# Performance work log

Measured on AMD Instinct MI355X. Metric: run time of the kernel, lower is better.

## Reference

```python
import jax, jax.numpy as jnp
import numpy as np

V, D, H, L, B, T = 32000, 1024, 16, 4, 2, 2048
DH = D // H
F = 4 * D
EPS = 1e-5


def setup_inputs() -> dict:
    key = jax.random.key(0)
    ks = jax.random.split(key, 16)
    s = 0.02
    n = lambda k, shape: (jax.random.normal(k, shape, jnp.float32) * s)
    inp = {
        "idx": jax.random.randint(ks[0], (B, T), 0, V, dtype=jnp.int64),
        "tok_emb": n(ks[1], (V, D)),
        "pos_emb": n(ks[2], (1, T, D)),
        # per-layer stacked params; Linear weights stored as (in, out)
        "Wq": n(ks[3], (L, D, D)), "bq": jnp.zeros((L, D)),
        "Wk": n(ks[4], (L, D, D)), "bk": jnp.zeros((L, D)),
        "Wv": n(ks[5], (L, D, D)), "bv": jnp.zeros((L, D)),
        "Wo": n(ks[6], (L, D, D)), "bo": jnp.zeros((L, D)),
        "ln1_g": jnp.ones((L, D)), "ln1_b": jnp.zeros((L, D)),
        "W1": n(ks[7], (L, D, F)), "b1": jnp.zeros((L, F)),
        "W2": n(ks[8], (L, F, D)), "b2": jnp.zeros((L, D)),
        "ln2_g": jnp.ones((L, D)), "ln2_b": jnp.zeros((L, D)),
        "lnf_g": jnp.ones((D,)), "lnf_b": jnp.zeros((D,)),
        "lm_W": n(ks[9], (D, V)),
    }
    return inp


def _ln(x, g, b):
    m = jnp.mean(x, axis=-1, keepdims=True)
    v = jnp.mean(jnp.square(x - m), axis=-1, keepdims=True)
    return (x - m) * jax.lax.rsqrt(v + EPS) * g + b


def _band_attn(x, Wq, bq, Wk, bk, Wv, bv, Wo, bo):
    # width-3 causal band: query t attends to keys {t, t-1, t-2}
    b_, t_, _ = x.shape
    q = (x @ Wq + bq).reshape(b_, t_, H, DH)
    k = (x @ Wk + bk).reshape(b_, t_, H, DH)
    v = (x @ Wv + bv).reshape(b_, t_, H, DH)

    def shift(a, o):  # align key at position t-o with query t
        return jnp.pad(a, ((0, 0), (o, 0), (0, 0), (0, 0)))[:, :t_]

    ks_ = jnp.stack([shift(k, o) for o in range(3)], axis=-2)  # (B,T,H,3,DH)
    vs_ = jnp.stack([shift(v, o) for o in range(3)], axis=-2)
    scale = 1.0 / np.sqrt(DH)
    scores = jnp.einsum('bthd,bthod->btho', q, ks_) * scale       # (B,T,H,3)
    pos = jnp.arange(t_)[None, :, None, None]
    off = jnp.arange(3)[None, None, None, :]
    scores = jnp.where(pos >= off, scores, -jnp.inf)
    p = jax.nn.softmax(scores, axis=-1)
    y = jnp.einsum('btho,bthod->bthd', p, vs_).reshape(b_, t_, D)
    return y @ Wo + bo


def reference(idx, tok_emb, pos_emb, Wq, bq, Wk, bk, Wv, bv, Wo, bo,
              ln1_g, ln1_b, W1, b1, W2, b2, ln2_g, ln2_b, lnf_g, lnf_b, lm_W):
    t_ = idx.shape[1]
    x = tok_emb[idx] + pos_emb[:, :t_, :]
    for i in range(L):
        h = _ln(x, ln1_g[i], ln1_b[i])
        x = x + _band_attn(h, Wq[i], bq[i], Wk[i], bk[i], Wv[i], bv[i], Wo[i], bo[i])
        h = _ln(x, ln2_g[i], ln2_b[i])
        h = jax.nn.gelu(h @ W1[i] + b1[i], approximate=False) @ W2[i] + b2[i]
        x = x + h
    x = _ln(x, lnf_g, lnf_b)
    logits = x @ lm_W
    return logits
```

## Files before the change

kernel.cpp:

```cpp
#include <hip/hip_runtime.h>
#include <cstdint>
#include <cstddef>

#define MROWS   4096
#define TSEQ    2048
#define DMODEL  1024
#define NHEAD   16
#define FFN     4096
#define NVOCAB  32000
#define NLAYER  4

typedef float  f32x4  __attribute__((ext_vector_type(4)));
typedef __bf16 bf16x8 __attribute__((ext_vector_type(8)));

#define VMCNT(n) asm volatile("s_waitcnt vmcnt(" #n ")" ::: "memory")
#define LGKM0()  asm volatile("s_waitcnt lgkmcnt(0)" ::: "memory")

__device__ __forceinline__ unsigned short f2bf(float f) {
    unsigned u = __builtin_bit_cast(unsigned, f);
    u += 0x7fffu + ((u >> 16) & 1u);
    return (unsigned short)(u >> 16);
}
__device__ __forceinline__ float bf2f(unsigned short u) {
    return __builtin_bit_cast(float, (unsigned)u << 16);
}

__device__ __forceinline__ float gelu_exact(float v) {
    return 0.5f * v * (1.0f + erff(v * 0.7071067811865476f));
}

__global__ __launch_bounds__(256) void embed_kernel(const int* __restrict__ idx,
                                                    const float* __restrict__ tok,
                                                    const float* __restrict__ pos,
                                                    float* __restrict__ x) {
    int row = blockIdx.x, tid = threadIdx.x;
    int token = idx[row];
    int t = row & (TSEQ - 1);
    float4 a = ((const float4*)(tok + (size_t)token * DMODEL))[tid];
    float4 p = ((const float4*)(pos + (size_t)t * DMODEL))[tid];
    a.x += p.x; a.y += p.y; a.z += p.z; a.w += p.w;
    ((float4*)(x + (size_t)row * DMODEL))[tid] = a;
}

__global__ __launch_bounds__(256) void ln_kernel(const float* __restrict__ x,
                                                 const float* __restrict__ g,
                                                 const float* __restrict__ b,
                                                 unsigned short* __restrict__ out) {
    int row = blockIdx.x, tid = threadIdx.x;
    float4 v = ((const float4*)(x + (size_t)row * DMODEL))[tid];
    float s1 = v.x + v.y + v.z + v.w;
    float s2 = v.x * v.x + v.y * v.y + v.z * v.z + v.w * v.w;
    for (int s = 32; s; s >>= 1) { s1 += __shfl_xor(s1, s); s2 += __shfl_xor(s2, s); }
    __shared__ float red[8];
    int lane = tid & 63, w = tid >> 6;
    if (lane == 0) { red[w] = s1; red[4 + w] = s2; }
    __syncthreads();
    s1 = red[0] + red[1] + red[2] + red[3];
    s2 = red[4] + red[5] + red[6] + red[7];
    float mean = s1 * (1.0f / DMODEL);
    float var  = s2 * (1.0f / DMODEL) - mean * mean;
    float rs   = rsqrtf(var + 1e-5f);
    float4 gv = ((const float4*)g)[tid];
    float4 bv = ((const float4*)b)[tid];
    size_t o = (size_t)row * DMODEL + tid * 4;
    out[o + 0] = f2bf((v.x - mean) * rs * gv.x + bv.x);
    out[o + 1] = f2bf((v.y - mean) * rs * gv.y + bv.y);
    out[o + 2] = f2bf((v.z - mean) * rs * gv.z + bv.z);
    out[o + 3] = f2bf((v.w - mean) * rs * gv.w + bv.w);
}

__global__ __launch_bounds__(256) void transpose_bf16(const float* __restrict__ W,
                                                      unsigned short* __restrict__ WT,
                                                      int K, int ldW) {
    __shared__ float tile[64][65];
    int n0 = blockIdx.x * 64, k0 = blockIdx.y * 64;
    int tid = threadIdx.x;
    int lr4 = tid & 15;
    int rw  = tid >> 4;
#pragma unroll
    for (int p = 0; p < 4; ++p) {
        int k = rw + p * 16;
        float4 v = *(const float4*)(W + (size_t)(k0 + k) * ldW + n0 + lr4 * 4);
        tile[k][lr4 * 4 + 0] = v.x;
        tile[k][lr4 * 4 + 1] = v.y;
        tile[k][lr4 * 4 + 2] = v.z;
        tile[k][lr4 * 4 + 3] = v.w;
    }
    __syncthreads();
    int kc = tid & 15;
    int nr = tid >> 4;
#pragma unroll
    for (int p = 0; p < 4; ++p) {
        int n = nr + p * 16;
        ushort4 o;
        o.x = f2bf(tile[kc * 4 + 0][n]);
        o.y = f2bf(tile[kc * 4 + 1][n]);
        o.z = f2bf(tile[kc * 4 + 2][n]);
        o.w = f2bf(tile[kc * 4 + 3][n]);
        *(ushort4*)(WT + (size_t)(n0 + n) * K + k0 + kc * 4) = o;
    }
}

__global__ __launch_bounds__(256) void transpose_qkv(const float* __restrict__ Wq,
                                                     const float* __restrict__ Wk,
                                                     const float* __restrict__ Wv,
                                                     unsigned short* __restrict__ WT) {
    __shared__ float tile[64][65];
    const float* W = (blockIdx.z == 0) ? Wq : (blockIdx.z == 1) ? Wk : Wv;
    unsigned short* dst = WT + (size_t)blockIdx.z * DMODEL * DMODEL;
    int n0 = blockIdx.x * 64, k0 = blockIdx.y * 64;
    int tid = threadIdx.x;
    int lr4 = tid & 15, rw = tid >> 4;
#pragma unroll
    for (int p = 0; p < 4; ++p) {
        int k = rw + p * 16;
        float4 v = *(const float4*)(W + (size_t)(k0 + k) * DMODEL + n0 + lr4 * 4);
        tile[k][lr4 * 4 + 0] = v.x;
        tile[k][lr4 * 4 + 1] = v.y;
        tile[k][lr4 * 4 + 2] = v.z;
        tile[k][lr4 * 4 + 3] = v.w;
    }
    __syncthreads();
    int kc = tid & 15, nr = tid >> 4;
#pragma unroll
    for (int p = 0; p < 4; ++p) {
        int n = nr + p * 16;
        ushort4 o;
        o.x = f2bf(tile[kc * 4 + 0][n]);
        o.y = f2bf(tile[kc * 4 + 1][n]);
        o.z = f2bf(tile[kc * 4 + 2][n]);
        o.w = f2bf(tile[kc * 4 + 3][n]);
        *(ushort4*)(dst + (size_t)(n0 + n) * DMODEL + k0 + kc * 4) = o;
    }
}

__global__ __launch_bounds__(256) void pack_qkv_bias(const float* __restrict__ bq,
                                                     const float* __restrict__ bk,
                                                     const float* __restrict__ bv,
                                                     float* __restrict__ dst) {
    int i = blockIdx.x * 256 + threadIdx.x;
    int l = i / 3072, c = i % 3072;
    float v = (c < 1024) ? bq[l * 1024 + c]
            : (c < 2048) ? bk[l * 1024 + c - 1024]
                         : bv[l * 1024 + c - 2048];
    dst[i] = v;
}

__global__ __launch_bounds__(256) void attn_kernel(const unsigned short* __restrict__ qkv,
                                                   unsigned short* __restrict__ y) {
    int wid  = (blockIdx.x * 256 + threadIdx.x) >> 6;
    int lane = threadIdx.x & 63;
    int h = wid & (NHEAD - 1);
    int row = wid >> 4;
    int t = row & (TSEQ - 1);
    const unsigned short* base = qkv + (size_t)row * 3072 + h * 64;
    float qd = bf2f(base[lane]);
    float d0 = qd * bf2f(base[1024 + lane]);
    float d1 = (t >= 1) ? qd * bf2f(base[1024 - 3072 + lane]) : 0.0f;
    float d2 = (t >= 2) ? qd * bf2f(base[1024 - 6144 + lane]) : 0.0f;
    for (int s = 32; s; s >>= 1) {
        d0 += __shfl_xor(d0, s); d1 += __shfl_xor(d1, s); d2 += __shfl_xor(d2, s);
    }
    d0 *= 0.125f; d1 *= 0.125f; d2 *= 0.125f;
    float m = d0;
    if (t >= 1) m = fmaxf(m, d1);
    if (t >= 2) m = fmaxf(m, d2);
    float p0 = expf(d0 - m);
    float p1 = (t >= 1) ? expf(d1 - m) : 0.0f;
    float p2 = (t >= 2) ? expf(d2 - m) : 0.0f;
    float den = p0 + p1 + p2;
    float v0 = bf2f(base[2048 + lane]);
    float v1 = (t >= 1) ? bf2f(base[2048 - 3072 + lane]) : 0.0f;
    float v2 = (t >= 2) ? bf2f(base[2048 - 6144 + lane]) : 0.0f;
    float yv = (p0 * v0 + p1 * v1 + p2 * v2) / den;
    y[(size_t)row * DMODEL + h * 64 + lane] = f2bf(yv);
}

template <int EPI>
__global__ __launch_bounds__(512, 2) void gemm256(const unsigned short* __restrict__ A,
                                                  const unsigned short* __restrict__ BT,
                                                  const float* __restrict__ bias,
                                                  const float* __restrict__ res,
                                                  float* __restrict__ outF,
                                                  unsigned short* __restrict__ outB,
                                                  int M, int N, int K, int ldc) {
    __shared__ unsigned short As[2][2][8192];
    __shared__ unsigned short Bs[2][2][8192];
    const int tid = threadIdx.x;
    const int lane = tid & 63, wid = tid >> 6;
    const int wr = wid >> 2, wc = wid & 3;
    const int lr = lane & 15, kq = lane >> 4;

    const int nbm = M >> 8;
    const int nwg = gridDim.x;
    int orig = blockIdx.x;
    int q8 = nwg >> 3, r8 = nwg & 7;
    int xcd = orig & 7, lin = orig >> 3;
    int wg = (xcd < r8 ? xcd * (q8 + 1) : r8 * (q8 + 1) + (xcd - r8) * q8) + lin;
    int bm = wg % nbm, bn = wg / nbm;

    const unsigned short* Ab = A + (size_t)bm * 256 * K;
    const unsigned short* Bb = BT + (size_t)bn * 256 * K;

    int sG0, sG1;
    {
        int pc0 = tid,        l0 = pc0 >> 3, s0 = pc0 & 7;
        int pc1 = 512 + tid,  l1 = pc1 >> 3, s1 = pc1 & 7;
        sG0 = (l0 * 2 + (s0 >> 2)) * K + (((s0 & 3) ^ (l0 & 3)) * 8);
        sG1 = (l1 * 2 + (s1 >> 2)) * K + (((s1 & 3) ^ (l1 & 3)) * 8);
    }

#define STAGE256(REGION, GBASE, TT, KH) do {                                                   \
    __builtin_amdgcn_global_load_lds(                                                          \
        (const __attribute__((address_space(1))) void*)((GBASE) + sG0 + (TT) * 64 + (KH) * 32),\
        (__attribute__((address_space(3))) void*)((REGION) + (size_t)tid * 8), 16, 0, 0);      \
    __builtin_amdgcn_global_load_lds(                                                          \
        (const __attribute__((address_space(1))) void*)((GBASE) + sG1 + (TT) * 64 + (KH) * 32),\
        (__attribute__((address_space(3))) void*)((REGION) + (size_t)(512 + tid) * 8), 16, 0, 0);\
} while (0)

    const int slot = ((lane & 1) << 2) | (kq ^ ((lr >> 1) & 3));
    const int laneOff = ((lr >> 1) << 6) + slot * 8;
    const int aBase = wr * 4096 + laneOff;
    const int bBase = wc * 2048 + laneOff;

    f32x4 acc[8][4] = {};
    const int nt = K >> 6;

    STAGE256(&As[0][0][0], Ab, 0, 0);
    STAGE256(&Bs[0][0][0], Bb, 0, 0);
    STAGE256(&As[0][1][0], Ab, 0, 1);
    STAGE256(&Bs[0][1][0], Bb, 0, 1);
    VMCNT(4);
    __builtin_amdgcn_s_barrier();

    for (int t = 0; t < nt; ++t) {
        const int buf = t & 1;
        const bool pf = (t + 1) < nt;
        const unsigned short* A0 = &As[buf][0][0];
        const unsigned short* A1 = &As[buf][1][0];
        const unsigned short* B0 = &Bs[buf][0][0];
        const unsigned short* B1 = &Bs[buf][1][0];
        unsigned short* nA0 = &As[buf ^ 1][0][0];
        unsigned short* nA1 = &As[buf ^ 1][1][0];
        unsigned short* nB0 = &Bs[buf ^ 1][0][0];
        unsigned short* nB1 = &Bs[buf ^ 1][1][0];

        bf16x8 a[8], b0, b1;

#pragma unroll
        for (int m = 0; m < 8; ++m) a[m] = *(const bf16x8*)(A0 + aBase + m * 512);
        b0 = *(const bf16x8*)(B0 + bBase + 0 * 512);
        b1 = *(const bf16x8*)(B0 + bBase + 1 * 512);
        if (pf) STAGE256(nA0, Ab, t + 1, 0);
        __builtin_amdgcn_s_barrier();
        LGKM0();
        __builtin_amdgcn_s_setprio(1);
#pragma unroll
        for (int m = 0; m < 8; ++m) {
            acc[m][0] = __builtin_amdgcn_mfma_f32_16x16x32_bf16(a[m], b0, acc[m][0], 0, 0, 0);
            acc[m][1] = __builtin_amdgcn_mfma_f32_16x16x32_bf16(a[m], b1, acc[m][1], 0, 0, 0);
        }
        __builtin_amdgcn_s_setprio(0);
        __builtin_amdgcn_s_barrier();

        b0 = *(const bf16x8*)(B0 + bBase + 2 * 512);
        b1 = *(const bf16x8*)(B0 + bBase + 3 * 512);
        if (pf) STAGE256(nB0, Bb, t + 1, 0);
        __builtin_amdgcn_s_barrier();
        LGKM0();
        __builtin_amdgcn_s_setprio(1);
#pragma unroll
        for (int m = 0; m < 8; ++m) {
            acc[m][2] = __builtin_amdgcn_mfma_f32_16x16x32_bf16(a[m], b0, acc[m][2], 0, 0, 0);
            acc[m][3] = __builtin_amdgcn_mfma_f32_16x16x32_bf16(a[m], b1, acc[m][3], 0, 0, 0);
        }
        __builtin_amdgcn_s_setprio(0);
        if (pf) VMCNT(4); else VMCNT(0);
        __builtin_amdgcn_s_barrier();

#pragma unroll
        for (int m = 0; m < 8; ++m) a[m] = *(const bf16x8*)(A1 + aBase + m * 512);
        b0 = *(const bf16x8*)(B1 + bBase + 0 * 512);
        b1 = *(const bf16x8*)(B1 + bBase + 1 * 512);
        if (pf) STAGE256(nA1, Ab, t + 1, 1);
        __builtin_amdgcn_s_barrier();
        LGKM0();
        __builtin_amdgcn_s_setprio(1);
#pragma unroll
        for (int m = 0; m < 8; ++m) {
            acc[m][0] = __builtin_amdgcn_mfma_f32_16x16x32_bf16(a[m], b0, acc[m][0], 0, 0, 0);
            acc[m][1] = __builtin_amdgcn_mfma_f32_16x16x32_bf16(a[m], b1, acc[m][1], 0, 0, 0);
        }
        __builtin_amdgcn_s_setprio(0);
        __builtin_amdgcn_s_barrier();

        b0 = *(const bf16x8*)(B1 + bBase + 2 * 512);
        b1 = *(const bf16x8*)(B1 + bBase + 3 * 512);
        if (pf) STAGE256(nB1, Bb, t + 1, 1);
        __builtin_amdgcn_s_barrier();
        LGKM0();
        __builtin_amdgcn_s_setprio(1);
#pragma unroll
        for (int m = 0; m < 8; ++m) {
            acc[m][2] = __builtin_amdgcn_mfma_f32_16x16x32_bf16(a[m], b0, acc[m][2], 0, 0, 0);
            acc[m][3] = __builtin_amdgcn_mfma_f32_16x16x32_bf16(a[m], b1, acc[m][3], 0, 0, 0);
        }
        __builtin_amdgcn_s_setprio(0);
        if (pf) VMCNT(4);
        __builtin_amdgcn_s_barrier();
    }

    const int row0 = bm * 256 + wr * 128;
    const int col0 = bn * 256 + wc * 64;
#pragma unroll
    for (int m = 0; m < 8; ++m) {
#pragma unroll
        for (int n = 0; n < 4; ++n) {
            int col = col0 + n * 16 + lr;
            int rbase = row0 + m * 16 + kq * 4;
            float bb = bias ? bias[col] : 0.0f;
#pragma unroll
            for (int j = 0; j < 4; ++j) {
                size_t off = (size_t)(rbase + j) * ldc + col;
                float v = acc[m][n][j] + bb;
                if (EPI == 1) v += res[off];
                if (EPI == 2)      outB[off] = f2bf(gelu_exact(v));
                else if (EPI == 3) outB[off] = f2bf(v);
                else               outF[off] = v;
            }
        }
    }
#undef STAGE256
}

template <int EPI>
__global__ __launch_bounds__(512, 4) void gemm128(const unsigned short* __restrict__ A,
                                                  const unsigned short* __restrict__ BT,
                                                  const float* __restrict__ bias,
                                                  const float* __restrict__ res,
                                                  float* __restrict__ outF,
                                                  unsigned short* __restrict__ outB,
                                                  int M, int N, int K, int ldc) {
    __shared__ unsigned short As[4][128 * 32];
    __shared__ unsigned short Bs[4][128 * 32];
    const int tid = threadIdx.x;
    const int lane = tid & 63, wid = tid >> 6;
    const int wr = wid >> 2, wc = wid & 3;
    const int lr = lane & 15, kq = lane >> 4;

    const int nbm = M >> 7;
    const int nwg = gridDim.x;
    int orig = blockIdx.x;
    int q8 = nwg >> 3, r8 = nwg & 7;
    int xcd = orig & 7, lin = orig >> 3;
    int wg = (xcd < r8 ? xcd * (q8 + 1) : r8 * (q8 + 1) + (xcd - r8) * q8) + lin;
    int bm = wg % nbm, bn = wg / nbm;

    const unsigned short* Ab = A + (size_t)bm * 128 * K;
    const unsigned short* Bb = BT + (size_t)bn * 128 * K;

    int sOff;
    {
        int l0 = tid >> 3, s0 = tid & 7;
        sOff = (l0 * 2 + (s0 >> 2)) * K + (((s0 & 3) ^ (l0 & 3)) * 8);
    }

#define STAGE_AB128(T) do {                                                                    \
    __builtin_amdgcn_global_load_lds(                                                          \
        (const __attribute__((address_space(1))) void*)(Ab + sOff + (T) * 32),                 \
        (__attribute__((address_space(3))) void*)(&As[(T) & 3][0] + (size_t)tid * 8), 16, 0, 0); \
    __builtin_amdgcn_global_load_lds(                                                          \
        (const __attribute__((address_space(1))) void*)(Bb + sOff + (T) * 32),                 \
        (__attribute__((address_space(3))) void*)(&Bs[(T) & 3][0] + (size_t)tid * 8), 16, 0, 0); \
} while (0)

    const int slot = ((lane & 1) << 2) | (kq ^ ((lr >> 1) & 3));
    const int laneOff = ((lr >> 1) << 6) + slot * 8;
    int aOff[4], bOff[2];
#pragma unroll
    for (int m = 0; m < 4; ++m) aOff[m] = wr * 2048 + m * 512 + laneOff;
#pragma unroll
    for (int n = 0; n < 2; ++n) bOff[n] = wc * 1024 + n * 512 + laneOff;

    f32x4 acc[4][2] = {};
    const int nt = K >> 5;

    STAGE_AB128(0); STAGE_AB128(1); STAGE_AB128(2);

#define GTILE128(T, WN, PF) do {                                                               \
    VMCNT(WN);                                                                                 \
    __builtin_amdgcn_s_barrier();                                                              \
    const unsigned short* sA_ = &As[(T) & 3][0];                                               \
    const unsigned short* sB_ = &Bs[(T) & 3][0];                                               \
    bf16x8 bfr[2], af[4];                                                                      \
    _Pragma("unroll") for (int n = 0; n < 2; ++n) bfr[n] = *(const bf16x8*)(sB_ + bOff[n]);    \
    _Pragma("unroll") for (int m = 0; m < 4; ++m) af[m] = *(const bf16x8*)(sA_ + aOff[m]);     \
    if (PF) STAGE_AB128((T) + 3);                                                              \
    __builtin_amdgcn_s_setprio(1);                                                             \
    _Pragma("unroll") for (int m = 0; m < 4; ++m)                                              \
        _Pragma("unroll") for (int n = 0; n < 2; ++n)                                          \
            acc[m][n] = __builtin_amdgcn_mfma_f32_16x16x32_bf16(af[m], bfr[n], acc[m][n], 0, 0, 0); \
    __builtin_amdgcn_s_setprio(0);                                                             \
} while (0)

    int t = 0;
    for (; t < nt - 3; ++t) GTILE128(t, 4, true);
    GTILE128(t, 4, false); ++t;
    GTILE128(t, 2, false); ++t;
    GTILE128(t, 0, false);

    const int row0 = bm * 128 + wr * 64;
    const int col0 = bn * 128 + wc * 32;
#pragma unroll
    for (int m = 0; m < 4; ++m) {
#pragma unroll
        for (int n = 0; n < 2; ++n) {
            int col = col0 + n * 16 + lr;
            int rbase = row0 + m * 16 + kq * 4;
            float bb = bias ? bias[col] : 0.0f;
#pragma unroll
            for (int j = 0; j < 4; ++j) {
                size_t off = (size_t)(rbase + j) * ldc + col;
                float v = acc[m][n][j] + bb;
                if (EPI == 1) v += res[off];
                if (EPI == 2)      outB[off] = f2bf(gelu_exact(v));
                else if (EPI == 3) outB[off] = f2bf(v);
                else               outF[off] = v;
            }
        }
    }
#undef GTILE128
#undef STAGE_AB128
}

extern "C" void kernel_launch(void* const* d_in, const int* in_sizes, int n_in,
                              void* d_out, int out_size, void* d_ws, size_t ws_size,
                              hipStream_t stream) {
    const int*   idx  = (const int*)d_in[0];
    const float* tok  = (const float*)d_in[1];
    const float* pos  = (const float*)d_in[2];
    const float* Wq   = (const float*)d_in[3];
    const float* bq   = (const float*)d_in[4];
    const float* Wk   = (const float*)d_in[5];
    const float* bk   = (const float*)d_in[6];
    const float* Wv   = (const float*)d_in[7];
    const float* bv   = (const float*)d_in[8];
    const float* Wo   = (const float*)d_in[9];
    const float* bo   = (const float*)d_in[10];
    const float* ln1g = (const float*)d_in[11];
    const float* ln1b = (const float*)d_in[12];
    const float* W1   = (const float*)d_in[13];
    const float* b1   = (const float*)d_in[14];
    const float* W2   = (const float*)d_in[15];
    const float* b2   = (const float*)d_in[16];
    const float* ln2g = (const float*)d_in[17];
    const float* ln2b = (const float*)d_in[18];
    const float* lnfg = (const float*)d_in[19];
    const float* lnfb = (const float*)d_in[20];
    const float* lmW  = (const float*)d_in[21];

    const bool bigws = ws_size >= (92ull << 20);

    char* ws = (char*)d_ws;
    unsigned short* wbuf;
    unsigned short* hbuf;
    unsigned short* ybuf;
    unsigned short* xfbuf;
    float*          bqkv;
    if (bigws) {
        wbuf  = (unsigned short*)(ws);
        hbuf  = (unsigned short*)(ws + (63ull << 20));
        ybuf  = (unsigned short*)(ws + (71ull << 20));
        xfbuf = (unsigned short*)(ws + (79ull << 20));
        bqkv  = (float*)(ws + (87ull << 20));
    } else {
        wbuf  = (unsigned short*)(ws);
        hbuf  = (unsigned short*)(ws + (16u << 20));
        ybuf  = (unsigned short*)(ws + (24u << 20));
        xfbuf = (unsigned short*)(ws + (32u << 20));
        bqkv  = (float*)(ws + (40u << 20));
    }

    float* outF = (float*)d_out;
    float* xbuf = outF;
    unsigned short* qkv = (unsigned short*)((char*)d_out + (16ull << 20));
    unsigned short* hidden = (unsigned short*)((char*)d_out + (64ull << 20));

    embed_kernel<<<MROWS, 256, 0, stream>>>(idx, tok, pos, xbuf);
    pack_qkv_bias<<<(NLAYER * 3072) / 256, 256, 0, stream>>>(bq, bk, bv, bqkv);

    for (int l = 0; l < NLAYER; l++) {
        const size_t wl = (size_t)l * DMODEL * DMODEL;
        ln_kernel<<<MROWS, 256, 0, stream>>>(xbuf, ln1g + l * DMODEL, ln1b + l * DMODEL, hbuf);

        transpose_qkv<<<dim3(16, 16, 3), 256, 0, stream>>>(Wq + wl, Wk + wl, Wv + wl, wbuf);
        gemm256<3><<<dim3((3072 / 256) * (MROWS / 256)), 512, 0, stream>>>(
            hbuf, wbuf, bqkv + l * 3072, nullptr, nullptr, qkv, MROWS, 3072, DMODEL, 3072);

        attn_kernel<<<MROWS * NHEAD / 4, 256, 0, stream>>>(qkv, ybuf);

        transpose_bf16<<<dim3(16, 16), 256, 0, stream>>>(Wo + wl, wbuf, DMODEL, DMODEL);
        gemm128<1><<<dim3((DMODEL / 128) * (MROWS / 128)), 512, 0, stream>>>(
            ybuf, wbuf, bo + l * DMODEL, xbuf, xbuf, nullptr, MROWS, DMODEL, DMODEL, DMODEL);

        ln_kernel<<<MROWS, 256, 0, stream>>>(xbuf, ln2g + l * DMODEL, ln2b + l * DMODEL, hbuf);

        transpose_bf16<<<dim3(FFN / 64, DMODEL / 64), 256, 0, stream>>>(W1 + (size_t)l * DMODEL * FFN, wbuf, DMODEL, FFN);
        gemm256<2><<<dim3((FFN / 256) * (MROWS / 256)), 512, 0, stream>>>(
            hbuf, wbuf, b1 + l * FFN, nullptr, nullptr, hidden, MROWS, FFN, DMODEL, FFN);

        transpose_bf16<<<dim3(DMODEL / 64, FFN / 64), 256, 0, stream>>>(W2 + (size_t)l * FFN * DMODEL, wbuf, FFN, DMODEL);
        gemm128<1><<<dim3((DMODEL / 128) * (MROWS / 128)), 512, 0, stream>>>(
            hidden, wbuf, b2 + l * DMODEL, xbuf, xbuf, nullptr, MROWS, DMODEL, FFN, DMODEL);
    }

    ln_kernel<<<MROWS, 256, 0, stream>>>(xbuf, lnfg, lnfb, xfbuf);

    if (bigws) {
        transpose_bf16<<<dim3(NVOCAB / 64, DMODEL / 64), 256, 0, stream>>>(lmW, wbuf, DMODEL, NVOCAB);
        gemm256<0><<<dim3((NVOCAB / 256) * (MROWS / 256)), 512, 0, stream>>>(
            xfbuf, wbuf, nullptr, nullptr, outF, nullptr, MROWS, NVOCAB, DMODEL, NVOCAB);
    } else {
        const int NCHUNK = 6400;
        for (int c = 0; c < NVOCAB / NCHUNK; c++) {
            int n0 = c * NCHUNK;
            transpose_bf16<<<dim3(NCHUNK / 64, DMODEL / 64), 256, 0, stream>>>(lmW + n0, wbuf, DMODEL, NVOCAB);
            gemm256<0><<<dim3((NCHUNK / 256) * (MROWS / 256)), 512, 0, stream>>>(
                xfbuf, wbuf, nullptr, nullptr, outF + n0, nullptr, MROWS, NCHUNK, DMODEL, NVOCAB);
        }
    }
}
```

Baseline: 1.331 ms.

## Replace gemm128 with 256-thread gemmv2 and split-K the W2 projection

Adds a new 128x128-tile GEMM kernel with 256 threads, a double-buffered LDS pipeline and a 4x4 MFMA tile per wave. It replaces gemm128 for the Wo projection and gemm256 for the W1+GELU projection. The W2 projection (K=4096) is split into two K halves that write fp32 partials, and a combine kernel then adds the bias and residual. The aim is more workgroups in flight and better occupancy on the narrow-N GEMMs. The cost is the extra partial-buffer traffic and one extra launch, and the double-buffered pipeline, with a barrier every k-step, may hide latency less well than the removed kernels.

```diff
diff --git a/kernel.cpp b/kernel.cpp
--- a/kernel.cpp
+++ b/kernel.cpp
@@ -146,6 +146,23 @@
     dst[i] = v;
 }
 
+__global__ __launch_bounds__(256) void combine2(const float* __restrict__ p0,
+                                                const float* __restrict__ p1,
+                                                const float* __restrict__ bias,
+                                                float* __restrict__ x) {
+    int i = blockIdx.x * 256 + threadIdx.x;
+    float4 a = ((const float4*)p0)[i];
+    float4 b = ((const float4*)p1)[i];
+    float4 xv = ((float4*)x)[i];
+    int col = (i * 4) & (DMODEL - 1);
+    float4 bb = *(const float4*)(bias + col);
+    xv.x += a.x + b.x + bb.x;
+    xv.y += a.y + b.y + bb.y;
+    xv.z += a.z + b.z + bb.z;
+    xv.w += a.w + b.w + bb.w;
+    ((float4*)x)[i] = xv;
+}
+
 __global__ __launch_bounds__(256) void attn_kernel(const unsigned short* __restrict__ qkv,
                                                    unsigned short* __restrict__ y) {
     int wid  = (blockIdx.x * 256 + threadIdx.x) >> 6;
@@ -177,6 +194,113 @@
 }
 
 template <int EPI>
+__global__ __launch_bounds__(256, 3) void gemmv2(const unsigned short* __restrict__ A,
+                                                 const unsigned short* __restrict__ BT,
+                                                 const float* __restrict__ bias,
+                                                 const float* __restrict__ res,
+                                                 float* __restrict__ outF,
+                                                 unsigned short* __restrict__ outB,
+                                                 int M, int N, int Ks, int KL, int ldc) {
+    __shared__ unsigned short As[2][4096];
+    __shared__ unsigned short Bs[2][4096];
+    const int tid = threadIdx.x;
+    const int lane = tid & 63, wid = tid >> 6;
+    const int wr = wid >> 1, wc = wid & 1;
+    const int lr = lane & 15, kq = lane >> 4;
+
+    const int nbm = M >> 7;
+    const int nwg = gridDim.x;
+    int orig = blockIdx.x;
+    int q8 = nwg >> 3, r8 = nwg & 7;
+    int xcd = orig & 7, lin = orig >> 3;
+    int wg = (xcd < r8 ? xcd * (q8 + 1) : r8 * (q8 + 1) + (xcd - r8) * q8) + lin;
+    int bm = wg % nbm, bn = wg / nbm;
+    const int kc = blockIdx.y;
+
+    const unsigned short* Ab = A + (size_t)bm * 128 * Ks + (size_t)kc * KL;
+    const unsigned short* Bb = BT + (size_t)bn * 128 * Ks + (size_t)kc * KL;
+
+    int sOff[2];
+#pragma unroll
+    for (int i = 0; i < 2; ++i) {
+        int pc = i * 256 + tid;
+        int line = pc >> 3, slot = pc & 7;
+        int row = line * 2 + (slot >> 2);
+        int c = (slot & 3) ^ (line & 3);
+        sOff[i] = row * Ks + c * 8;
+    }
+
+#define STAGEV2(T) do {                                                                        \
+    unsigned short* dA_ = &As[(T) & 1][0];                                                     \
+    unsigned short* dB_ = &Bs[(T) & 1][0];                                                     \
+    _Pragma("unroll") for (int i_ = 0; i_ < 2; ++i_) {                                         \
+        __builtin_amdgcn_global_load_lds(                                                      \
+            (const __attribute__((address_space(1))) void*)(Ab + sOff[i_] + (T) * 32),         \
+            (__attribute__((address_space(3))) void*)(dA_ + (size_t)(i_ * 256 + tid) * 8), 16, 0, 0); \
+        __builtin_amdgcn_global_load_lds(                                                      \
+            (const __attribute__((address_space(1))) void*)(Bb + sOff[i_] + (T) * 32),         \
+            (__attribute__((address_space(3))) void*)(dB_ + (size_t)(i_ * 256 + tid) * 8), 16, 0, 0); \
+    }                                                                                          \
+} while (0)
+
+    const int slot = ((lane & 1) << 2) | (kq ^ ((lr >> 1) & 3));
+    const int laneOff = ((lr >> 1) << 6) + slot * 8;
+    int aOff[4], bOff[4];
+#pragma unroll
+    for (int m = 0; m < 4; ++m) aOff[m] = wr * 2048 + m * 512 + laneOff;
+#pragma unroll
+    for (int n = 0; n < 4; ++n) bOff[n] = wc * 2048 + n * 512 + laneOff;
+
+    f32x4 acc[4][4] = {};
+    const int nt = KL >> 5;
+
+    STAGEV2(0);
+    __syncthreads();
+
+    for (int t = 0; t < nt; ++t) {
+        const bool pf = (t + 1) < nt;
+        if (pf) STAGEV2(t + 1);
+        const unsigned short* sA = &As[t & 1][0];
+        const unsigned short* sB = &Bs[t & 1][0];
+        bf16x8 a[4], b[4];
+#pragma unroll
+        for (int m = 0; m < 4; ++m) a[m] = *(const bf16x8*)(sA + aOff[m]);
+#pragma unroll
+        for (int n = 0; n < 4; ++n) b[n] = *(const bf16x8*)(sB + bOff[n]);
+        __builtin_amdgcn_s_setprio(1);
+#pragma unroll
+        for (int m = 0; m < 4; ++m)
+#pragma unroll
+            for (int n = 0; n < 4; ++n)
+                acc[m][n] = __builtin_amdgcn_mfma_f32_16x16x32_bf16(a[m], b[n], acc[m][n], 0, 0, 0);
+        __builtin_amdgcn_s_setprio(0);
+        if (pf) __syncthreads();
+    }
+
+    const int row0 = bm * 128 + wr * 64;
+    const int col0 = bn * 128 + wc * 64;
+    float* outP = (EPI == 0) ? (outF + (size_t)kc * M * ldc) : outF;
+#pragma unroll
+    for (int m = 0; m < 4; ++m) {
+#pragma unroll
+        for (int n = 0; n < 4; ++n) {
+            int col = col0 + n * 16 + lr;
+            int rbase = row0 + m * 16 + kq * 4;
+            float bb = (EPI != 0 && bias) ? bias[col] : 0.0f;
+#pragma unroll
+            for (int j = 0; j < 4; ++j) {
+                size_t off = (size_t)(rbase + j) * ldc + col;
+                float v = acc[m][n][j] + bb;
+                if (EPI == 1) v += res[off];
+                if (EPI == 2)      outB[off] = f2bf(gelu_exact(v));
+                else               outP[off] = v;
+            }
+        }
+    }
+#undef STAGEV2
+}
+
+template <int EPI>
 __global__ __launch_bounds__(512, 2) void gemm256(const unsigned short* __restrict__ A,
                                                   const unsigned short* __restrict__ BT,
                                                   const float* __restrict__ bias,
@@ -332,106 +456,6 @@
         }
     }
 #undef STAGE256
-}
-
-template <int EPI>
-__global__ __launch_bounds__(512, 4) void gemm128(const unsigned short* __restrict__ A,
-                                                  const unsigned short* __restrict__ BT,
-                                                  const float* __restrict__ bias,
-                                                  const float* __restrict__ res,
-                                                  float* __restrict__ outF,
-                                                  unsigned short* __restrict__ outB,
-                                                  int M, int N, int K, int ldc) {
-    __shared__ unsigned short As[4][128 * 32];
-    __shared__ unsigned short Bs[4][128 * 32];
-    const int tid = threadIdx.x;
-    const int lane = tid & 63, wid = tid >> 6;
-    const int wr = wid >> 2, wc = wid & 3;
-    const int lr = lane & 15, kq = lane >> 4;
-
-    const int nbm = M >> 7;
-    const int nwg = gridDim.x;
-    int orig = blockIdx.x;
-    int q8 = nwg >> 3, r8 = nwg & 7;
-    int xcd = orig & 7, lin = orig >> 3;
-    int wg = (xcd < r8 ? xcd * (q8 + 1) : r8 * (q8 + 1) + (xcd - r8) * q8) + lin;
-    int bm = wg % nbm, bn = wg / nbm;
-
-    const unsigned short* Ab = A + (size_t)bm * 128 * K;
-    const unsigned short* Bb = BT + (size_t)bn * 128 * K;
-
-    int sOff;
-    {
-        int l0 = tid >> 3, s0 = tid & 7;
-        sOff = (l0 * 2 + (s0 >> 2)) * K + (((s0 & 3) ^ (l0 & 3)) * 8);
-    }
-
-#define STAGE_AB128(T) do {                                                                    \
-    __builtin_amdgcn_global_load_lds(                                                          \
-        (const __attribute__((address_space(1))) void*)(Ab + sOff + (T) * 32),                 \
-        (__attribute__((address_space(3))) void*)(&As[(T) & 3][0] + (size_t)tid * 8), 16, 0, 0); \
-    __builtin_amdgcn_global_load_lds(                                                          \
-        (const __attribute__((address_space(1))) void*)(Bb + sOff + (T) * 32),                 \
-        (__attribute__((address_space(3))) void*)(&Bs[(T) & 3][0] + (size_t)tid * 8), 16, 0, 0); \
-} while (0)
-
-    const int slot = ((lane & 1) << 2) | (kq ^ ((lr >> 1) & 3));
-    const int laneOff = ((lr >> 1) << 6) + slot * 8;
-    int aOff[4], bOff[2];
-#pragma unroll
-    for (int m = 0; m < 4; ++m) aOff[m] = wr * 2048 + m * 512 + laneOff;
-#pragma unroll
-    for (int n = 0; n < 2; ++n) bOff[n] = wc * 1024 + n * 512 + laneOff;
-
-    f32x4 acc[4][2] = {};
-    const int nt = K >> 5;
-
-    STAGE_AB128(0); STAGE_AB128(1); STAGE_AB128(2);
-
-#define GTILE128(T, WN, PF) do {                                                               \
-    VMCNT(WN);                                                                                 \
-    __builtin_amdgcn_s_barrier();                                                              \
-    const unsigned short* sA_ = &As[(T) & 3][0];                                               \
-    const unsigned short* sB_ = &Bs[(T) & 3][0];                                               \
-    bf16x8 bfr[2], af[4];                                                                      \
-    _Pragma("unroll") for (int n = 0; n < 2; ++n) bfr[n] = *(const bf16x8*)(sB_ + bOff[n]);    \
-    _Pragma("unroll") for (int m = 0; m < 4; ++m) af[m] = *(const bf16x8*)(sA_ + aOff[m]);     \
-    if (PF) STAGE_AB128((T) + 3);                                                              \
-    __builtin_amdgcn_s_setprio(1);                                                             \
-    _Pragma("unroll") for (int m = 0; m < 4; ++m)                                              \
-        _Pragma("unroll") for (int n = 0; n < 2; ++n)                                          \
-            acc[m][n] = __builtin_amdgcn_mfma_f32_16x16x32_bf16(af[m], bfr[n], acc[m][n], 0, 0, 0); \
-    __builtin_amdgcn_s_setprio(0);                                                             \
-} while (0)
-
-    int t = 0;
-    for (; t < nt - 3; ++t) GTILE128(t, 4, true);
-    GTILE128(t, 4, false); ++t;
-    GTILE128(t, 2, false); ++t;
-    GTILE128(t, 0, false);
-
-    const int row0 = bm * 128 + wr * 64;
-    const int col0 = bn * 128 + wc * 32;
-#pragma unroll
-    for (int m = 0; m < 4; ++m) {
-#pragma unroll
-        for (int n = 0; n < 2; ++n) {
-            int col = col0 + n * 16 + lr;
-            int rbase = row0 + m * 16 + kq * 4;
-            float bb = bias ? bias[col] : 0.0f;
-#pragma unroll
-            for (int j = 0; j < 4; ++j) {
-                size_t off = (size_t)(rbase + j) * ldc + col;
-                float v = acc[m][n][j] + bb;
-                if (EPI == 1) v += res[off];
-                if (EPI == 2)      outB[off] = f2bf(gelu_exact(v));
-                else if (EPI == 3) outB[off] = f2bf(v);
-                else               outF[off] = v;
-            }
-        }
-    }
-#undef GTILE128
-#undef STAGE_AB128
 }
 
 extern "C" void kernel_launch(void* const* d_in, const int* in_sizes, int n_in,
@@ -486,6 +510,7 @@
     float* xbuf = outF;
     unsigned short* qkv = (unsigned short*)((char*)d_out + (16ull << 20));
     unsigned short* hidden = (unsigned short*)((char*)d_out + (64ull << 20));
+    float* pbuf = (float*)((char*)d_out + (96ull << 20));
 
     embed_kernel<<<MROWS, 256, 0, stream>>>(idx, tok, pos, xbuf);
     pack_qkv_bias<<<(NLAYER * 3072) / 256, 256, 0, stream>>>(bq, bk, bv, bqkv);
@@ -501,18 +526,20 @@
         attn_kernel<<<MROWS * NHEAD / 4, 256, 0, stream>>>(qkv, ybuf);
 
         transpose_bf16<<<dim3(16, 16), 256, 0, stream>>>(Wo + wl, wbuf, DMODEL, DMODEL);
-        gemm128<1><<<dim3((DMODEL / 128) * (MROWS / 128)), 512, 0, stream>>>(
-            ybuf, wbuf, bo + l * DMODEL, xbuf, xbuf, nullptr, MROWS, DMODEL, DMODEL, DMODEL);
+        gemmv2<1><<<dim3((MROWS / 128) * (DMODEL / 128), 1), 256, 0, stream>>>(
+            ybuf, wbuf, bo + l * DMODEL, xbuf, xbuf, nullptr, MROWS, DMODEL, DMODEL, DMODEL, DMODEL);
 
         ln_kernel<<<MROWS, 256, 0, stream>>>(xbuf, ln2g + l * DMODEL, ln2b + l * DMODEL, hbuf);
 
         transpose_bf16<<<dim3(FFN / 64, DMODEL / 64), 256, 0, stream>>>(W1 + (size_t)l * DMODEL * FFN, wbuf, DMODEL, FFN);
-        gemm256<2><<<dim3((FFN / 256) * (MROWS / 256)), 512, 0, stream>>>(
-            hbuf, wbuf, b1 + l * FFN, nullptr, nullptr, hidden, MROWS, FFN, DMODEL, FFN);
+        gemmv2<2><<<dim3((MROWS / 128) * (FFN / 128), 1), 256, 0, stream>>>(
+            hbuf, wbuf, b1 + l * FFN, nullptr, nullptr, hidden, MROWS, FFN, DMODEL, DMODEL, FFN);
 
         transpose_bf16<<<dim3(DMODEL / 64, FFN / 64), 256, 0, stream>>>(W2 + (size_t)l * FFN * DMODEL, wbuf, FFN, DMODEL);
-        gemm128<1><<<dim3((DMODEL / 128) * (MROWS / 128)), 512, 0, stream>>>(
-            hidden, wbuf, b2 + l * DMODEL, xbuf, xbuf, nullptr, MROWS, DMODEL, FFN, DMODEL);
+        gemmv2<0><<<dim3((MROWS / 128) * (DMODEL / 128), 2), 256, 0, stream>>>(
+            hidden, wbuf, nullptr, nullptr, pbuf, nullptr, MROWS, DMODEL, FFN, FFN / 2, DMODEL);
+        combine2<<<MROWS * DMODEL / 4 / 256, 256, 0, stream>>>(
+            pbuf, pbuf + (size_t)MROWS * DMODEL, b2 + l * DMODEL, xbuf);
     }
 
     ln_kernel<<<MROWS, 256, 0, stream>>>(xbuf, lnfg, lnfb, xfbuf);
```

Result: no change. 1.322 ms (-0.7%).
